# Performance work log

Measured on AMD Instinct MI355X. Metric: run time of the kernel, lower is better.

The kernel has to match this reference:

```python
import jax, jax.numpy as jnp
import numpy as np

N_NODES = 100000


def gcn_conv(x, edge_index, W, b, n_nodes):
    # PyG GCNConv: h = x @ W; add self-loops; symmetric normalization; aggregate to dst; + bias
    h = x @ W  # [N, out]
    loop = jnp.arange(n_nodes, dtype=edge_index.dtype)
    src = jnp.concatenate([edge_index[0], loop])
    dst = jnp.concatenate([edge_index[1], loop])
    ones = jnp.ones(src.shape[0], dtype=h.dtype)
    deg = jax.ops.segment_sum(ones, dst, num_segments=n_nodes)  # in-degree incl. self-loop
    dinv = jnp.where(deg > 0, jax.lax.rsqrt(deg), 0.0)
    norm = dinv[src] * dinv[dst]  # [E+N]
    msgs = h[src] * norm[:, None]  # gather + scale
    out = jax.ops.segment_sum(msgs, dst, num_segments=n_nodes)  # scatter-add
    return out + b


def setup_inputs() -> dict:
    key = jax.random.key(0)
    k1, k2, k3, k4 = jax.random.split(key, 4)
    x = jax.random.normal(k1, (N_NODES, 256), dtype=jnp.float32)
    edge_index = jax.random.randint(k2, (2, 3200000), 0, N_NODES, dtype=jnp.int64)
    W1 = jax.random.normal(k3, (256, 64), dtype=jnp.float32) * (1.0 / np.sqrt(256))
    b1 = jnp.zeros((64,), dtype=jnp.float32)
    W2 = jax.random.normal(k4, (64, 40), dtype=jnp.float32) * (1.0 / np.sqrt(64))
    b2 = jnp.zeros((40,), dtype=jnp.float32)
    return {"x": x, "edge_index": edge_index, "W1": W1, "b1": b1, "W2": W2, "b2": b2}


def reference(x, edge_index, W1, b1, W2, b2):
    n = x.shape[0]
    h = gcn_conv(x, edge_index, W1, b1, n)
    h = jax.nn.relu(h)
    h = gcn_conv(h, edge_index, W2, b2, n)
    return jax.nn.log_softmax(h, axis=1)
```

## Files before the change

### kernel.cpp

```cpp
#include <hip/hip_runtime.h>
#include <hip/hip_bf16.h>
#include <math.h>

static constexpr int NN    = 100000;
static constexpr int BSH   = 9;
static constexpr int NBUCK = (NN + 511) >> 9;
static constexpr int EPB   = 8192;
static constexpr int CAP   = 24576;

typedef __attribute__((ext_vector_type(8))) short short8;
typedef __attribute__((ext_vector_type(4))) float f32x4;
typedef __attribute__((ext_vector_type(2))) float f32x2;

#if defined(__has_builtin)
#  if __has_builtin(__builtin_amdgcn_cvt_pk_f32_fp8) && __has_builtin(__builtin_amdgcn_cvt_pk_fp8_f32)
#    define USE_HW_FP8 1
#  endif
#endif
#ifndef USE_HW_FP8
#  define USE_HW_FP8 0
#endif

__device__ __forceinline__ short f2bf(float f) {
    __hip_bfloat16 h = __float2bfloat16(f);
    return __builtin_bit_cast(short, h);
}

__device__ __forceinline__ float fp8_dec_sw(unsigned b) {
    unsigned u = ((b & 0x80u) << 24) | ((b & 0x7Fu) << 20);
    return __builtin_bit_cast(float, u) * 0x1p120f;
}
__device__ __forceinline__ unsigned fp8_enc_sw(float f) {
    unsigned u = __builtin_bit_cast(unsigned, f * 0x1p-120f);
    unsigned s = (u >> 24) & 0x80u;
    unsigned mag = u & 0x7FFFFFFFu;
    unsigned t = mag + 0x7FFFFu + ((mag >> 20) & 1u);
    unsigned r = t >> 20;
    if (r > 0x7Eu) r = 0x7Eu;
    return s | r;
}

template<bool HI>
__device__ __forceinline__ f32x2 dec2w(unsigned u) {
#if USE_HW_FP8
    return __builtin_amdgcn_cvt_pk_f32_fp8(u, HI);
#else
    unsigned w = HI ? (u >> 16) : u;
    f32x2 r;
    r.x = fp8_dec_sw(w & 0xFFu);
    r.y = fp8_dec_sw((w >> 8) & 0xFFu);
    return r;
#endif
}
__device__ __forceinline__ unsigned enc2(float a, float b) {
#if USE_HW_FP8
    return (unsigned)__builtin_amdgcn_cvt_pk_fp8_f32(a, b, 0, false);
#else
    return fp8_enc_sw(a) | (fp8_enc_sw(b) << 8);
#endif
}

__device__ __forceinline__ void acc8(f32x2* a, uint2 u) {
    a[0] += dec2w<false>(u.x);
    a[1] += dec2w<true>(u.x);
    a[2] += dec2w<false>(u.y);
    a[3] += dec2w<true>(u.y);
}
__device__ __forceinline__ void acc8s(f32x2* a, uint2 u, float ds) {
    f32x2 w = {ds, ds};
    a[0] = dec2w<false>(u.x) * w + a[0];
    a[1] = dec2w<true>(u.x)  * w + a[1];
    a[2] = dec2w<false>(u.y) * w + a[2];
    a[3] = dec2w<true>(u.y)  * w + a[3];
}

__device__ __forceinline__ long long ldidx(const void* __restrict__ p, long long i, int is64) {
    if (is64) return ((const long long* __restrict__)p)[i];
    return (long long)((const int* __restrict__)p)[i];
}

template<int K, int NCOLS, int KT, int NT>
__device__ __forceinline__ void packB_dev(const float* __restrict__ W,
                                          short* __restrict__ P, int t) {
    if (t >= KT * NT * 64) return;
    int kt = t / (NT * 64);
    int nt = (t / 64) % NT;
    int l  = t & 63;
    int g  = l >> 4;
#pragma unroll
    for (int e = 0; e < 8; ++e) {
        int k   = kt * 32 + g * 8 + e;
        int col = nt * 16 + (l & 15);
        float v = (col < NCOLS) ? W[k * NCOLS + col] : 0.0f;
        P[t * 8 + e] = f2bf(v);
    }
}

__global__ void __launch_bounds__(256)
k_init(const unsigned int* __restrict__ e32, int* __restrict__ flag,
       int* __restrict__ gcur,
       const float* __restrict__ W1, short* __restrict__ pB1,
       const float* __restrict__ W2, short* __restrict__ pB2) {
    int blk = blockIdx.x, tid = threadIdx.x;
    if (blk == 0) {
        if (tid < NBUCK) gcur[tid] = 0;
        __shared__ int any_nz;
        if (tid == 0) any_nz = 0;
        __syncthreads();
        unsigned int nz = 0;
        for (int w = 1 + 2 * tid; w < 4096; w += 512)
            nz |= e32[w];
        if (nz) atomicOr(&any_nz, 1);
        __syncthreads();
        if (tid == 0) *flag = (any_nz == 0) ? 1 : 0;
    } else if (blk <= 8) {
        packB_dev<256, 64, 8, 4>(W1, pB1, (blk - 1) * 256 + tid);
    } else {
        packB_dev<64, 40, 2, 3>(W2, pB2, (blk - 9) * 256 + tid);
    }
}

__global__ void __launch_bounds__(1024)
k_build_gemm1(const void* __restrict__ eidx, const int* __restrict__ flag, long long E,
              int nsblk, int ngblk, int* __restrict__ gcur, unsigned* __restrict__ ebuf,
              const float* __restrict__ X, const short* __restrict__ pB1,
              unsigned char* __restrict__ H, int n) {
    int bid = (int)blockIdx.x;
    int mn = nsblk < ngblk ? nsblk : ngblk;
    int role, idx;
    if (bid < 2 * mn) { role = bid & 1; idx = bid >> 1; }
    else {
        int rem = bid - 2 * mn;
        role = (nsblk > ngblk) ? 0 : 1;
        idx = mn + rem;
    }
    if (role == 0) {
        __shared__ int h[NBUCK];
        for (int b = threadIdx.x; b < NBUCK; b += 1024) h[b] = 0;
        __syncthreads();
        int is64 = *flag;
        long long base = (long long)idx * EPB;
        long long end  = base + EPB < E ? base + EPB : E;
        unsigned sv[8], dv[8];
        bool ok[8];
#pragma unroll
        for (int k = 0; k < 8; ++k) {
            long long e = base + (long long)k * 1024 + threadIdx.x;
            ok[k] = (e < end);
            if (ok[k]) {
                sv[k] = (unsigned)ldidx(eidx, e, is64);
                dv[k] = (unsigned)ldidx(eidx, E + e, is64);
                atomicAdd(&h[dv[k] >> BSH], 1);
            }
        }
        __syncthreads();
        for (int b = threadIdx.x; b < NBUCK; b += 1024)
            h[b] = atomicAdd(&gcur[b], h[b]);
        __syncthreads();
#pragma unroll
        for (int k = 0; k < 8; ++k) {
            if (ok[k]) {
                int bk = dv[k] >> BSH;
                int pos = atomicAdd(&h[bk], 1);
                ebuf[(long long)bk * CAP + pos] = sv[k] | ((dv[k] & 511u) << 17);
            }
        }
    } else {
        __shared__ alignas(16) short sW[8 * 4 * 512];
        __shared__ alignas(16) short sX[64 * 264];
        short8* dst = (short8*)sW;
        const short8* src = (const short8*)pB1;
        int tid = threadIdx.x;
        for (int i = tid; i < 2048; i += 1024) dst[i] = src[i];

        int wave = tid >> 6, lane = tid & 63;
        int g   = lane >> 4;
        int wig = wave >> 2;
        int nt  = wave & 3;

        int lr = tid >> 4;
        int c0 = (tid & 15) * 16;

        for (int s = 0; s < 4; ++s) {
            int grow = idx * 256 + s * 64 + lr;
            short8 lo, hi;
            if (grow < n) {
                const float* xr = X + (long long)grow * 256 + c0;
                float4 u0 = *(const float4*)(xr);
                float4 u1 = *(const float4*)(xr + 4);
                float4 u2 = *(const float4*)(xr + 8);
                float4 u3 = *(const float4*)(xr + 12);
                lo[0] = f2bf(u0.x); lo[1] = f2bf(u0.y); lo[2] = f2bf(u0.z); lo[3] = f2bf(u0.w);
                lo[4] = f2bf(u1.x); lo[5] = f2bf(u1.y); lo[6] = f2bf(u1.z); lo[7] = f2bf(u1.w);
                hi[0] = f2bf(u2.x); hi[1] = f2bf(u2.y); hi[2] = f2bf(u2.z); hi[3] = f2bf(u2.w);
                hi[4] = f2bf(u3.x); hi[5] = f2bf(u3.y); hi[6] = f2bf(u3.z); hi[7] = f2bf(u3.w);
            } else {
                lo = (short8){0,0,0,0,0,0,0,0};
                hi = lo;
            }
            __syncthreads();
            *(short8*)&sX[lr * 264 + c0]     = lo;
            *(short8*)&sX[lr * 264 + c0 + 8] = hi;
            __syncthreads();

            f32x4 acc = (f32x4){0.f, 0.f, 0.f, 0.f};
            const short* arow_p = &sX[(wig * 16 + (lane & 15)) * 264];
#pragma unroll
            for (int kt = 0; kt < 8; ++kt) {
                short8 a = *(const short8*)(arow_p + kt * 32 + g * 8);
                short8 bfr = dst[(kt * 4 + nt) * 64 + lane];
                acc = __builtin_amdgcn_mfma_f32_16x16x32_bf16(a, bfr, acc, 0, 0, 0);
            }
            int c = nt * 16 + (lane & 15);
            int orow_base = idx * 256 + s * 64 + wig * 16 + g * 4;
#pragma unroll
            for (int r = 0; r < 4; ++r) {
                int orow = orow_base + r;
                if (orow < n)
                    H[(long long)orow * 64 + c] =
                        (unsigned char)(enc2(acc[r], 0.0f) & 0xFFu);
            }
        }
    }
}

__global__ void __launch_bounds__(1024)
k_bucket_csr(const unsigned* __restrict__ ebuf, const int* __restrict__ gcnt,
             int* __restrict__ rowst, float* __restrict__ dinv,
             int* __restrict__ csr, int n) {
    __shared__ int cnt[512];
    __shared__ int cursor[512];
    __shared__ int woff[8];
    __shared__ int bs_sh;
    int b = blockIdx.x;
    int t = threadIdx.x;
    int cb = gcnt[b];
    long long rbase = (long long)b * CAP;
    if (t == 0) bs_sh = 0;
    if (t < 512) cnt[t] = 0;
    __syncthreads();
    if (t < b) atomicAdd(&bs_sh, gcnt[t]);
    for (int i = t; i < cb; i += 1024) {
        unsigned ed = ebuf[rbase + i];
        atomicAdd(&cnt[ed >> 17], 1);
    }
    __syncthreads();
    int bs = bs_sh;
    if (b == NBUCK - 1 && t == 0) rowst[n] = bs + cb;
    int v = 0, ps = 0;
    if (t < 512) {
        v = cnt[t];
        ps = v;
        int lane = t & 63;
#pragma unroll
        for (int off = 1; off < 64; off <<= 1) {
            int up = __shfl_up(ps, off);
            if (lane >= off) ps += up;
        }
        if (lane == 63) woff[t >> 6] = ps;
    }
    __syncthreads();
    if (t == 0) {
        int run = 0;
#pragma unroll
        for (int i = 0; i < 8; ++i) { int x = woff[i]; woff[i] = run; run += x; }
    }
    __syncthreads();
    if (t < 512) {
        int incl  = ps + woff[t >> 6];
        int start = bs + incl - v;
        int gnode = (b << BSH) + t;
        if (gnode < n) {
            rowst[gnode] = start;
            dinv[gnode]  = rsqrtf((float)(v + 1));
        }
        cursor[t] = start;
    }
    __syncthreads();
    for (int i = t; i < cb; i += 1024) {
        unsigned ed = ebuf[rbase + i];
        int pos = atomicAdd(&cursor[ed >> 17], 1);
        csr[pos] = (int)(ed & 0x1FFFFu);
    }
}

template<int K, int NCOLS, int KT, int NT, bool ABF16>
__global__ void __launch_bounds__(256)
k_mfma_gemm(const void* __restrict__ Xv, const short* __restrict__ packedB,
            const float* __restrict__ dinv, unsigned char* __restrict__ H, int n) {
    __shared__ alignas(16) short sW[KT * NT * 512];
    short8* dst = (short8*)sW;
    const short8* src = (const short8*)packedB;
    constexpr int TOT8 = KT * NT * 64;
    for (int i = threadIdx.x; i < TOT8; i += 256) dst[i] = src[i];
    __syncthreads();

    int wave = threadIdx.x >> 6, lane = threadIdx.x & 63;
    int g = lane >> 4;
    int arow = blockIdx.x * 64 + wave * 16 + (lane & 15);

    f32x4 acc[NT];
#pragma unroll
    for (int nt = 0; nt < NT; ++nt) acc[nt] = (f32x4){0.f, 0.f, 0.f, 0.f};

#pragma unroll
    for (int kt = 0; kt < KT; ++kt) {
        short8 a;
        if (arow < n) {
            int k0 = kt * 32 + g * 8;
            if (ABF16) {
                const short* xr = (const short*)Xv + (long long)arow * K;
                a = *(const short8*)(xr + k0);
            } else {
                const float* xr = (const float*)Xv + (long long)arow * K;
                float4 u = *(const float4*)(xr + k0);
                float4 v = *(const float4*)(xr + k0 + 4);
                a[0] = f2bf(u.x); a[1] = f2bf(u.y); a[2] = f2bf(u.z); a[3] = f2bf(u.w);
                a[4] = f2bf(v.x); a[5] = f2bf(v.y); a[6] = f2bf(v.z); a[7] = f2bf(v.w);
            }
        } else {
            a = (short8){0, 0, 0, 0, 0, 0, 0, 0};
        }
#pragma unroll
        for (int nt = 0; nt < NT; ++nt) {
            short8 bfr = dst[(kt * NT + nt) * 64 + lane];
            acc[nt] = __builtin_amdgcn_mfma_f32_16x16x32_bf16(a, bfr, acc[nt], 0, 0, 0);
        }
    }

    int c = lane & 15;
    int orow_base = blockIdx.x * 64 + wave * 16 + g * 4;
#pragma unroll
    for (int r = 0; r < 4; ++r) {
        int orow = orow_base + r;
        if (orow < n) {
            float di = dinv[orow];
            float v[NT];
#pragma unroll
            for (int nt = 0; nt < NT; ++nt) v[nt] = acc[nt][r] * di;
            unsigned char* hp = H + (long long)orow * NCOLS;
#pragma unroll
            for (int p = 0; p < NT; p += 2) {
                unsigned wrd = enc2(v[p], (p + 1 < NT) ? v[p + 1] : 0.0f);
                int col0 = p * 16 + c;
                if (col0 < NCOLS) hp[col0] = (unsigned char)(wrd & 0xFFu);
                if (p + 1 < NT) {
                    int col1 = col0 + 16;
                    if (col1 < NCOLS) hp[col1] = (unsigned char)((wrd >> 8) & 0xFFu);
                }
            }
        }
    }
}

__global__ void __launch_bounds__(256)
k_gather_relu(const int* __restrict__ rowst, const int* __restrict__ csr,
              const unsigned char* __restrict__ h1s, const float* __restrict__ dinv,
              const float* __restrict__ b, unsigned short* __restrict__ out, int n) {
    long long gid = (long long)blockIdx.x * blockDim.x + threadIdx.x;
    int node = (int)(gid >> 3);
    int fe   = (int)(gid & 7);
    if (node >= n) return;
    int jb = rowst[node], je = rowst[node + 1];
    unsigned feoff = (unsigned)fe << 3;

    f32x2 a0[4], a1[4], a2[4], a3[4];
#pragma unroll
    for (int q = 0; q < 4; ++q) {
        a0[q] = (f32x2){0.f, 0.f}; a1[q] = (f32x2){0.f, 0.f};
        a2[q] = (f32x2){0.f, 0.f}; a3[q] = (f32x2){0.f, 0.f};
    }

    int j = jb;
    for (; j + 3 < je; j += 4) {
        int s0 = csr[j], s1 = csr[j + 1], s2 = csr[j + 2], s3 = csr[j + 3];
        float ds0 = dinv[s0], ds1 = dinv[s1], ds2 = dinv[s2], ds3 = dinv[s3];
        uint2 u0 = *(const uint2*)(h1s + (((unsigned)s0 << 6) + feoff));
        uint2 u1 = *(const uint2*)(h1s + (((unsigned)s1 << 6) + feoff));
        uint2 u2 = *(const uint2*)(h1s + (((unsigned)s2 << 6) + feoff));
        uint2 u3 = *(const uint2*)(h1s + (((unsigned)s3 << 6) + feoff));
        acc8s(a0, u0, ds0);
        acc8s(a1, u1, ds1);
        acc8s(a2, u2, ds2);
        acc8s(a3, u3, ds3);
    }
    for (; j < je; ++j) {
        int s0 = csr[j];
        float ds0 = dinv[s0];
        uint2 u0 = *(const uint2*)(h1s + (((unsigned)s0 << 6) + feoff));
        acc8s(a0, u0, ds0);
    }
#pragma unroll
    for (int q = 0; q < 4; ++q) a0[q] += (a1[q] + a2[q]) + a3[q];

    float dn = dinv[node];
    uint2 self = *(const uint2*)(h1s + (((unsigned)node << 6) + feoff));
    acc8s(a0, self, dn);
    unsigned short r[8];
#pragma unroll
    for (int q = 0; q < 4; ++q) {
        float v0 = fmaxf(a0[q].x * dn + b[8 * fe + 2 * q],     0.0f);
        float v1 = fmaxf(a0[q].y * dn + b[8 * fe + 2 * q + 1], 0.0f);
        r[2 * q]     = (unsigned short)f2bf(v0);
        r[2 * q + 1] = (unsigned short)f2bf(v1);
    }
    uint4 pk;
    pk.x = (unsigned)r[0] | ((unsigned)r[1] << 16);
    pk.y = (unsigned)r[2] | ((unsigned)r[3] << 16);
    pk.z = (unsigned)r[4] | ((unsigned)r[5] << 16);
    pk.w = (unsigned)r[6] | ((unsigned)r[7] << 16);
    ((uint4*)(out + (long long)node * 64))[fe] = pk;
}

__global__ void __launch_bounds__(256)
k_gather_lsm(const int* __restrict__ rowst, const int* __restrict__ csr,
             const unsigned char* __restrict__ h2s, const float* __restrict__ dinv,
             const float* __restrict__ b, float* __restrict__ out, int n) {
    long long gid = (long long)blockIdx.x * blockDim.x + threadIdx.x;
    int node = (int)(gid >> 3);
    int fe   = (int)(gid & 7);
    if (node >= n) return;
    bool act = (fe < 5);
    int jb = rowst[node], je = rowst[node + 1];
    unsigned feoff = (unsigned)fe << 3;

    f32x2 a0[4], a1[4], a2[4], a3[4];
#pragma unroll
    for (int q = 0; q < 4; ++q) {
        a0[q] = (f32x2){0.f, 0.f}; a1[q] = (f32x2){0.f, 0.f};
        a2[q] = (f32x2){0.f, 0.f}; a3[q] = (f32x2){0.f, 0.f};
    }

    int j = jb;
    for (; j + 3 < je; j += 4) {
        int s0 = csr[j], s1 = csr[j + 1], s2 = csr[j + 2], s3 = csr[j + 3];
        if (act) {
            uint2 u0 = *(const uint2*)(h2s + ((unsigned)s0 * 40u + feoff));
            uint2 u1 = *(const uint2*)(h2s + ((unsigned)s1 * 40u + feoff));
            uint2 u2 = *(const uint2*)(h2s + ((unsigned)s2 * 40u + feoff));
            uint2 u3 = *(const uint2*)(h2s + ((unsigned)s3 * 40u + feoff));
            acc8(a0, u0);
            acc8(a1, u1);
            acc8(a2, u2);
            acc8(a3, u3);
        }
    }
    for (; j < je; ++j) {
        int s0 = csr[j];
        if (act) {
            uint2 u0 = *(const uint2*)(h2s + ((unsigned)s0 * 40u + feoff));
            acc8(a0, u0);
        }
    }
#pragma unroll
    for (int q = 0; q < 4; ++q) a0[q] += (a1[q] + a2[q]) + a3[q];

    float va[8];
    float mloc = -INFINITY;
    if (act) {
        uint2 self = *(const uint2*)(h2s + ((unsigned)node * 40u + feoff));
        acc8(a0, self);
        float di = dinv[node];
#pragma unroll
        for (int q = 0; q < 4; ++q) {
            va[2 * q]     = a0[q].x * di + b[8 * fe + 2 * q];
            va[2 * q + 1] = a0[q].y * di + b[8 * fe + 2 * q + 1];
            mloc = fmaxf(mloc, fmaxf(va[2 * q], va[2 * q + 1]));
        }
    }
    float m = mloc;
    m = fmaxf(m, __shfl_xor(m, 1));
    m = fmaxf(m, __shfl_xor(m, 2));
    m = fmaxf(m, __shfl_xor(m, 4));
    float ex = 0.0f;
    if (act) {
#pragma unroll
        for (int k = 0; k < 8; ++k) ex += __expf(va[k] - m);
    }
    ex += __shfl_xor(ex, 1);
    ex += __shfl_xor(ex, 2);
    ex += __shfl_xor(ex, 4);
    float lse = __logf(ex);
    if (act) {
        float4 r0 = make_float4(va[0] - m - lse, va[1] - m - lse,
                                va[2] - m - lse, va[3] - m - lse);
        float4 r1 = make_float4(va[4] - m - lse, va[5] - m - lse,
                                va[6] - m - lse, va[7] - m - lse);
        *(float4*)(out + (long long)node * 40 + 8 * fe)     = r0;
        *(float4*)(out + (long long)node * 40 + 8 * fe + 4) = r1;
    }
}

extern "C" void kernel_launch(void* const* d_in, const int* in_sizes, int n_in,
                              void* d_out, int out_size, void* d_ws, size_t ws_size,
                              hipStream_t stream) {
    const float* x  = (const float*)d_in[0];
    const void*  ei = d_in[1];
    const float* W1 = (const float*)d_in[2];
    const float* b1 = (const float*)d_in[3];
    const float* W2 = (const float*)d_in[4];
    const float* b2 = (const float*)d_in[5];
    float* out = (float*)d_out;

    const long long E = (long long)in_sizes[1] / 2;
    const int nsblk = (int)((E + EPB - 1) / EPB);
    const int ngblk = (NN + 255) / 256;

    char* w = (char*)d_ws;
    auto alloc = [&](size_t bytes) -> void* {
        void* p = (void*)w;
        w += (bytes + 255) & ~(size_t)255;
        return p;
    };
    int*      flag    = (int*)     alloc(4);
    int*      gcur    = (int*)     alloc((size_t)NBUCK * 4);
    int*      rowst   = (int*)     alloc(((size_t)NN + 1) * 4);
    float*    dinv    = (float*)   alloc((size_t)NN * 4);
    short*    pB1     = (short*)   alloc((size_t)8 * 4 * 64 * 8 * 2);
    short*    pB2     = (short*)   alloc((size_t)2 * 3 * 64 * 8 * 2);
    int*      csr     = (int*)     alloc((size_t)E * 4);
    unsigned* ebuf    = (unsigned*)alloc((size_t)NBUCK * CAP * 4);
    unsigned char* h1s = (unsigned char*)alloc((size_t)NN * 64);
    unsigned short* agg1 = (unsigned short*)alloc((size_t)NN * 64 * 2);
    unsigned char* h2s = h1s;

    const int B = 256;
    auto cdiv = [](long long a, long long b) { return (int)((a + b - 1) / b); };

    k_init<<<11, B, 0, stream>>>((const unsigned int*)ei, flag, gcur, W1, pB1, W2, pB2);

    k_build_gemm1<<<nsblk + ngblk, 1024, 0, stream>>>(ei, flag, E, nsblk, ngblk,
                                                      gcur, ebuf, x, pB1, h1s, NN);

    k_bucket_csr<<<NBUCK, 1024, 0, stream>>>(ebuf, gcur, rowst, dinv, csr, NN);

    k_gather_relu<<<cdiv((long long)NN * 8, B), B, 0, stream>>>(rowst, csr, h1s, dinv, b1, agg1, NN);

    k_mfma_gemm<64, 40, 2, 3, true><<<cdiv(NN, 64), B, 0, stream>>>(agg1, pB2, dinv, h2s, NN);

    k_gather_lsm<<<cdiv((long long)NN * 8, B), B, 0, stream>>>(rowst, csr, h2s, dinv, b2, out, NN);
}
```

Before: 179.2 us.

## Split node edge lists across two thread groups and cache bucket edges in registers

Both gather kernels now assign 16 threads per node instead of 8. Two edge groups take alternating edges and are combined with a cross-lane shuffle reduction, which doubles memory-level parallelism for the latency-bound neighbour gathers at the cost of twice as many threads and extra shuffles. The bucket CSR kernel now keeps each thread's edge words in a 24-entry register array across both passes instead of re-reading the global buffer in the second pass. This raises register pressure and depends on CAP/1024 being 24.

```diff
diff --git a/kernel.cpp b/kernel.cpp
--- a/kernel.cpp
+++ b/kernel.cpp
@@ -240,9 +240,14 @@
     if (t < 512) cnt[t] = 0;
     __syncthreads();
     if (t < b) atomicAdd(&bs_sh, gcnt[t]);
-    for (int i = t; i < cb; i += 1024) {
-        unsigned ed = ebuf[rbase + i];
-        atomicAdd(&cnt[ed >> 17], 1);
+    unsigned ev[24];
+#pragma unroll
+    for (int k = 0; k < 24; ++k) {
+        int i = t + k * 1024;
+        if (i < cb) {
+            ev[k] = ebuf[rbase + i];
+            atomicAdd(&cnt[ev[k] >> 17], 1);
+        }
     }
     __syncthreads();
     int bs = bs_sh;
@@ -277,10 +282,13 @@
         cursor[t] = start;
     }
     __syncthreads();
-    for (int i = t; i < cb; i += 1024) {
-        unsigned ed = ebuf[rbase + i];
-        int pos = atomicAdd(&cursor[ed >> 17], 1);
-        csr[pos] = (int)(ed & 0x1FFFFu);
+#pragma unroll
+    for (int k = 0; k < 24; ++k) {
+        int i = t + k * 1024;
+        if (i < cb) {
+            int pos = atomicAdd(&cursor[ev[k] >> 17], 1);
+            csr[pos] = (int)(ev[k] & 0x1FFFFu);
+        }
     }
 }
 
@@ -358,8 +366,10 @@
               const unsigned char* __restrict__ h1s, const float* __restrict__ dinv,
               const float* __restrict__ b, unsigned short* __restrict__ out, int n) {
     long long gid = (long long)blockIdx.x * blockDim.x + threadIdx.x;
-    int node = (int)(gid >> 3);
-    int fe   = (int)(gid & 7);
+    int node = (int)(gid >> 4);
+    int sub  = (int)(gid & 15);
+    int eg   = sub >> 3;
+    int fe   = sub & 7;
     if (node >= n) return;
     int jb = rowst[node], je = rowst[node + 1];
     unsigned feoff = (unsigned)fe << 3;
@@ -371,9 +381,9 @@
         a2[q] = (f32x2){0.f, 0.f}; a3[q] = (f32x2){0.f, 0.f};
     }
 
-    int j = jb;
-    for (; j + 3 < je; j += 4) {
-        int s0 = csr[j], s1 = csr[j + 1], s2 = csr[j + 2], s3 = csr[j + 3];
+    int j = jb + eg;
+    for (; j + 6 < je; j += 8) {
+        int s0 = csr[j], s1 = csr[j + 2], s2 = csr[j + 4], s3 = csr[j + 6];
         float ds0 = dinv[s0], ds1 = dinv[s1], ds2 = dinv[s2], ds3 = dinv[s3];
         uint2 u0 = *(const uint2*)(h1s + (((unsigned)s0 << 6) + feoff));
         uint2 u1 = *(const uint2*)(h1s + (((unsigned)s1 << 6) + feoff));
@@ -384,7 +394,7 @@
         acc8s(a2, u2, ds2);
         acc8s(a3, u3, ds3);
     }
-    for (; j < je; ++j) {
+    for (; j < je; j += 2) {
         int s0 = csr[j];
         float ds0 = dinv[s0];
         uint2 u0 = *(const uint2*)(h1s + (((unsigned)s0 << 6) + feoff));
@@ -393,23 +403,31 @@
 #pragma unroll
     for (int q = 0; q < 4; ++q) a0[q] += (a1[q] + a2[q]) + a3[q];
 
-    float dn = dinv[node];
-    uint2 self = *(const uint2*)(h1s + (((unsigned)node << 6) + feoff));
-    acc8s(a0, self, dn);
-    unsigned short r[8];
 #pragma unroll
     for (int q = 0; q < 4; ++q) {
-        float v0 = fmaxf(a0[q].x * dn + b[8 * fe + 2 * q],     0.0f);
-        float v1 = fmaxf(a0[q].y * dn + b[8 * fe + 2 * q + 1], 0.0f);
-        r[2 * q]     = (unsigned short)f2bf(v0);
-        r[2 * q + 1] = (unsigned short)f2bf(v1);
-    }
-    uint4 pk;
-    pk.x = (unsigned)r[0] | ((unsigned)r[1] << 16);
-    pk.y = (unsigned)r[2] | ((unsigned)r[3] << 16);
-    pk.z = (unsigned)r[4] | ((unsigned)r[5] << 16);
-    pk.w = (unsigned)r[6] | ((unsigned)r[7] << 16);
-    ((uint4*)(out + (long long)node * 64))[fe] = pk;
+        a0[q].x += __shfl_xor(a0[q].x, 8);
+        a0[q].y += __shfl_xor(a0[q].y, 8);
+    }
+
+    if (eg == 0) {
+        float dn = dinv[node];
+        uint2 self = *(const uint2*)(h1s + (((unsigned)node << 6) + feoff));
+        acc8s(a0, self, dn);
+        unsigned short r[8];
+#pragma unroll
+        for (int q = 0; q < 4; ++q) {
+            float v0 = fmaxf(a0[q].x * dn + b[8 * fe + 2 * q],     0.0f);
+            float v1 = fmaxf(a0[q].y * dn + b[8 * fe + 2 * q + 1], 0.0f);
+            r[2 * q]     = (unsigned short)f2bf(v0);
+            r[2 * q + 1] = (unsigned short)f2bf(v1);
+        }
+        uint4 pk;
+        pk.x = (unsigned)r[0] | ((unsigned)r[1] << 16);
+        pk.y = (unsigned)r[2] | ((unsigned)r[3] << 16);
+        pk.z = (unsigned)r[4] | ((unsigned)r[5] << 16);
+        pk.w = (unsigned)r[6] | ((unsigned)r[7] << 16);
+        ((uint4*)(out + (long long)node * 64))[fe] = pk;
+    }
 }
 
 __global__ void __launch_bounds__(256)
@@ -417,8 +435,10 @@
              const unsigned char* __restrict__ h2s, const float* __restrict__ dinv,
              const float* __restrict__ b, float* __restrict__ out, int n) {
     long long gid = (long long)blockIdx.x * blockDim.x + threadIdx.x;
-    int node = (int)(gid >> 3);
-    int fe   = (int)(gid & 7);
+    int node = (int)(gid >> 4);
+    int sub  = (int)(gid & 15);
+    int eg   = sub >> 3;
+    int fe   = sub & 7;
     if (node >= n) return;
     bool act = (fe < 5);
     int jb = rowst[node], je = rowst[node + 1];
@@ -431,9 +451,9 @@
         a2[q] = (f32x2){0.f, 0.f}; a3[q] = (f32x2){0.f, 0.f};
     }
 
-    int j = jb;
-    for (; j + 3 < je; j += 4) {
-        int s0 = csr[j], s1 = csr[j + 1], s2 = csr[j + 2], s3 = csr[j + 3];
+    int j = jb + eg;
+    for (; j + 6 < je; j += 8) {
+        int s0 = csr[j], s1 = csr[j + 2], s2 = csr[j + 4], s3 = csr[j + 6];
         if (act) {
             uint2 u0 = *(const uint2*)(h2s + ((unsigned)s0 * 40u + feoff));
             uint2 u1 = *(const uint2*)(h2s + ((unsigned)s1 * 40u + feoff));
@@ -445,7 +465,7 @@
             acc8(a3, u3);
         }
     }
-    for (; j < je; ++j) {
+    for (; j < je; j += 2) {
         int s0 = csr[j];
         if (act) {
             uint2 u0 = *(const uint2*)(h2s + ((unsigned)s0 * 40u + feoff));
@@ -454,6 +474,12 @@
     }
 #pragma unroll
     for (int q = 0; q < 4; ++q) a0[q] += (a1[q] + a2[q]) + a3[q];
+
+#pragma unroll
+    for (int q = 0; q < 4; ++q) {
+        a0[q].x += __shfl_xor(a0[q].x, 8);
+        a0[q].y += __shfl_xor(a0[q].y, 8);
+    }
 
     float va[8];
     float mloc = -INFINITY;
@@ -472,16 +498,18 @@
     m = fmaxf(m, __shfl_xor(m, 1));
     m = fmaxf(m, __shfl_xor(m, 2));
     m = fmaxf(m, __shfl_xor(m, 4));
+    m = fmaxf(m, __shfl_xor(m, 8));
     float ex = 0.0f;
-    if (act) {
+    if (act && eg == 0) {
 #pragma unroll
         for (int k = 0; k < 8; ++k) ex += __expf(va[k] - m);
     }
     ex += __shfl_xor(ex, 1);
     ex += __shfl_xor(ex, 2);
     ex += __shfl_xor(ex, 4);
+    ex += __shfl_xor(ex, 8);
     float lse = __logf(ex);
-    if (act) {
+    if (act && eg == 0) {
         float4 r0 = make_float4(va[0] - m - lse, va[1] - m - lse,
                                 va[2] - m - lse, va[3] - m - lse);
         float4 r1 = make_float4(va[4] - m - lse, va[5] - m - lse,
@@ -534,9 +562,9 @@
 
     k_bucket_csr<<<NBUCK, 1024, 0, stream>>>(ebuf, gcur, rowst, dinv, csr, NN);
 
-    k_gather_relu<<<cdiv((long long)NN * 8, B), B, 0, stream>>>(rowst, csr, h1s, dinv, b1, agg1, NN);
+    k_gather_relu<<<cdiv((long long)NN * 16, B), B, 0, stream>>>(rowst, csr, h1s, dinv, b1, agg1, NN);
 
     k_mfma_gemm<64, 40, 2, 3, true><<<cdiv(NN, 64), B, 0, stream>>>(agg1, pB2, dinv, h2s, NN);
 
-    k_gather_lsm<<<cdiv((long long)NN * 8, B), B, 0, stream>>>(rowst, csr, h2s, dinv, b2, out, NN);
-}
+    k_gather_lsm<<<cdiv((long long)NN * 16, B), B, 0, stream>>>(rowst, csr, h2s, dinv, b2, out, NN);
+}
```

Result: faster. 174.8 us (-2.5%).
